# Optimization experiments

Hardware: AMD Instinct MI355X
Metric: run time of the kernel (lower is better)

Reference implementation:

```python
import jax, jax.numpy as jnp
import numpy as np
import math

B, H, S, D = 2, 16, 2048, 64

def setup_inputs() -> dict:
    key = jax.random.key(0)
    kq, kk, kv = jax.random.split(key, 3)
    Q = jax.random.normal(kq, (B, H, S, D), dtype=jnp.float32)
    K = jax.random.normal(kk, (B, H, S, D), dtype=jnp.float32)
    V = jax.random.normal(kv, (B, H, S, D), dtype=jnp.float32)
    causal_mask = jnp.tril(jnp.ones((S, S), dtype=bool))
    return {"Q": Q, "K": K, "V": V, "causal_mask": causal_mask}

def reference(Q, K, V, causal_mask):
    d_k = K.shape[-1]
    scores = jnp.einsum('bhqd,bhkd->bhqk', Q, K) / math.sqrt(d_k)
    scores = jnp.where(causal_mask, scores, -jnp.inf)
    probs = jax.nn.softmax(scores, axis=-1)
    return jnp.einsum('bhqk,bhkd->bhqd', probs, V)
```

## Files before the change

kernel.cpp:

```cpp
#include <hip/hip_runtime.h>
#include <math.h>


constexpr int kS   = 2048;
constexpr int kD   = 64;
constexpr int kBH  = 32;
constexpr int kPadP = 72;

typedef short short8 __attribute__((ext_vector_type(8)));
typedef float float4v __attribute__((ext_vector_type(4)));
typedef float float16v __attribute__((ext_vector_type(16)));
typedef unsigned int u32;
typedef unsigned short u16;

static __device__ inline u16 f2bf(float f) {
  union { float f; unsigned u; } v; v.f = f;
  unsigned r = v.u + 0x7FFF + ((v.u >> 16) & 1);
  return (u16)(r >> 16);
}

static __device__ inline short8 pack8(float4v a, float4v b) {
  short8 r;
  r[0] = (short)f2bf(a[0]); r[1] = (short)f2bf(a[1]);
  r[2] = (short)f2bf(a[2]); r[3] = (short)f2bf(a[3]);
  r[4] = (short)f2bf(b[0]); r[5] = (short)f2bf(b[1]);
  r[6] = (short)f2bf(b[2]); r[7] = (short)f2bf(b[3]);
  return r;
}

static __device__ inline void async_cp16(const void* g, void* l) {
  __builtin_amdgcn_global_load_lds(
      (const __attribute__((address_space(1))) u32*)g,
      (__attribute__((address_space(3))) u32*)l, 16, 0, 0);
}

static __device__ inline void xhalf(u32 pga, u32 pgb, u32& lo, u32& hi) {
#if __has_builtin(__builtin_amdgcn_permlane32_swap)
  auto r = __builtin_amdgcn_permlane32_swap(pga, pgb, false, false);
  lo = r[0];
  hi = r[1];
#else
  const u32 ea = (u32)__shfl_xor((int)pga, 32);
  const u32 eb = (u32)__shfl_xor((int)pgb, 32);
  const bool top = (threadIdx.x & 32) != 0;
  lo = top ? eb : pga;
  hi = top ? pgb : ea;
#endif
}

__global__ __launch_bounds__(256)
void prep_kernel(const float* __restrict__ Q, const float* __restrict__ K,
                 const float* __restrict__ V,
                 u16* __restrict__ Qb, u16* __restrict__ Kb, u16* __restrict__ VT) {
  __shared__ u16 tile[64 * kPadP];
  const int tid = threadIdx.x;
  const int bh = blockIdx.y, st = blockIdx.x;
  const size_t ibase = (size_t)bh * kS * kD + (size_t)st * 64 * kD;
  const int r  = tid >> 2;
  const int c0 = (tid & 3) * 16;
  {
    const float scl = 0.125f * 1.44269504089f;
    const float* qp = Q + ibase + (size_t)r * kD + c0;
    float4v a = *(const float4v*)(qp);
    float4v b = *(const float4v*)(qp + 4);
    float4v c = *(const float4v*)(qp + 8);
    float4v d = *(const float4v*)(qp + 12);
    #pragma unroll
    for (int i = 0; i < 4; ++i) { a[i] *= scl; b[i] *= scl; c[i] *= scl; d[i] *= scl; }
    u16* dst = Qb + ibase + (size_t)r * kD + c0;
    *(short8*)dst       = pack8(a, b);
    *(short8*)(dst + 8) = pack8(c, d);
  }
  {
    const float* kp = K + ibase + (size_t)r * kD + c0;
    float4v a = *(const float4v*)(kp);
    float4v b = *(const float4v*)(kp + 4);
    float4v c = *(const float4v*)(kp + 8);
    float4v d = *(const float4v*)(kp + 12);
    u16* dst = Kb + ibase + (size_t)r * kD + c0;
    *(short8*)dst       = pack8(a, b);
    *(short8*)(dst + 8) = pack8(c, d);
  }
  {
    const float* vp = V + ibase + (size_t)r * kD + c0;
    float4v a = *(const float4v*)(vp);
    float4v b = *(const float4v*)(vp + 4);
    float4v c = *(const float4v*)(vp + 8);
    float4v d = *(const float4v*)(vp + 12);
    u16* t = &tile[r * kPadP + c0];
    *(short8*)t       = pack8(a, b);
    *(short8*)(t + 8) = pack8(c, d);
  }
  __syncthreads();
  {
    const int dd = tid >> 2;
    const int s0 = (tid & 3) * 16;
    short8 w0, w1;
    #pragma unroll
    for (int i = 0; i < 8; ++i) {
      w0[i] = (short)tile[(s0 + i) * kPadP + dd];
      w1[i] = (short)tile[(s0 + 8 + i) * kPadP + dd];
    }
    u16* vdst = VT + (size_t)bh * kD * kS + (size_t)dd * kS + st * 64 + s0;
    *(short8*)vdst       = w0;
    *(short8*)(vdst + 8) = w1;
  }
}

__global__ __launch_bounds__(256, 2)
void fattn_kernel(const u16* __restrict__ Qb, const u16* __restrict__ Kb,
                  const u16* __restrict__ VT,
                  u32* __restrict__ O0, u32* __restrict__ O1,
                  u32* __restrict__ O2, u32* __restrict__ O3,
                  float* __restrict__ Lp) {
  __shared__ __align__(16) u16 ldsK[2][4096];
  __shared__ __align__(16) u16 ldsV[2][4096];

  const int tid  = threadIdx.x;
  const int wave = tid >> 6;
  const int lane = tid & 63;
  const int l31  = lane & 31;
  const int h    = lane >> 5;

  const int bh = blockIdx.y;
  const int p  = blockIdx.x >> 2;
  const int z  = blockIdx.x & 3;
  const int qiA = p, qiB = 7 - p;
  const int nA  = 4 * p + 4;

  const size_t base  = (size_t)bh * kS * kD;
  const size_t vbase = (size_t)bh * kD * kS;

  const int lr  = lane >> 3;
  const int cxl = (lane & 7) ^ lr;
  const int offK0 = lr * 64   + cxl * 8;
  const int offV0 = lr * 2048 + cxl * 8;
  const unsigned hs16 = ((unsigned)(h ^ (l31 & 7))) * 16;

  u32* Od = (z == 0) ? O0 : (z == 1) ? O1 : (z == 2) ? O2 : O3;
  const int cB = 9 * z;
  const int cE = cB + 9;

  short8 ones;
  #pragma unroll
  for (int i = 0; i < 8; ++i) ones[i] = (short)0x3F80;

  int par = 0;
  for (int seg = 0; seg < 2; ++seg) {
    const int qi = seg ? qiB : qiA;
    int tb, te;
    if (seg == 0) { tb = min(cB, nA); te = min(cE, nA); }
    else          { tb = max(cB, nA) - nA; te = max(cE, nA) - nA; }
    const int wq0 = qi * 256 + wave * 64;

    short8 qf[2][4];
    #pragma unroll
    for (int g = 0; g < 2; ++g) {
      const u16* qp = Qb + base + (size_t)(wq0 + 32 * g + l31) * kD + h * 8;
      #pragma unroll
      for (int dk = 0; dk < 4; ++dk) qf[g][dk] = *(const short8*)(qp + dk * 16);
    }

    float16v acc[2][2], lacc[2];
    #pragma unroll
    for (int g = 0; g < 2; ++g) {
      #pragma unroll
      for (int i = 0; i < 16; ++i) { acc[g][0][i] = 0.f; acc[g][1][i] = 0.f; lacc[g][i] = 0.f; }
    }

    if (tb < te) {
      {
        const u16* kg0 = Kb + base + (size_t)tb * 4096;
        const u16* vg0 = VT + vbase + tb * 64;
        const int b = par & 1;
        #pragma unroll
        for (int j = 0; j < 2; ++j) {
          const int g = wave + 4 * j;
          async_cp16(kg0 + g * 512 + offK0,           &ldsK[b][g * 512]);
          async_cp16(vg0 + (size_t)g * 16384 + offV0, &ldsV[b][g * 512]);
        }
      }
      for (int t = tb; t < te; ++t, ++par) {
        __syncthreads();
        if (t + 1 < te) {
          const u16* kg0 = Kb + base + (size_t)(t + 1) * 4096;
          const u16* vg0 = VT + vbase + (t + 1) * 64;
          const int b = (par + 1) & 1;
          #pragma unroll
          for (int j = 0; j < 2; ++j) {
            const int g = wave + 4 * j;
            async_cp16(kg0 + g * 512 + offK0,           &ldsK[b][g * 512]);
            async_cp16(vg0 + (size_t)g * 16384 + offV0, &ldsV[b][g * 512]);
          }
        }
        const char* KB = (const char*)ldsK[par & 1];
        const char* VB = (const char*)ldsV[par & 1];
        #pragma unroll
        for (int kt32 = 0; kt32 < 2; ++kt32) {
          const int ktb = t * 64 + kt32 * 32;
          if (ktb > wq0 + 63) break;
          const bool live0 = (ktb <= wq0 + 31);

          const char* krow = KB + (kt32 * 32 + l31) * 128;
          short8 kf[4];
          #pragma unroll
          for (int dk = 0; dk < 4; ++dk)
            kf[dk] = *(const short8*)(krow + (((unsigned)(dk * 32)) ^ hs16));
          short8 vf[4];
          #pragma unroll
          for (int c = 0; c < 2; ++c) {
            const unsigned coff = ((unsigned)((kt32 * 4 + 2 * c) * 16)) ^ hs16;
            vf[2 * c]     = *(const short8*)(VB + l31 * 128 + coff);
            vf[2 * c + 1] = *(const short8*)(VB + (32 + l31) * 128 + coff);
          }

          float16v s0, s1;
          #pragma unroll
          for (int i = 0; i < 16; ++i) { s0[i] = 0.f; s1[i] = 0.f; }
          if (live0) {
            #pragma unroll
            for (int dk = 0; dk < 4; ++dk)
              s0 = __builtin_amdgcn_mfma_f32_32x32x16_bf16(kf[dk], qf[0][dk], s0, 0, 0, 0);
          }
          #pragma unroll
          for (int dk = 0; dk < 4; ++dk)
            s1 = __builtin_amdgcn_mfma_f32_32x32x16_bf16(kf[dk], qf[1][dk], s1, 0, 0, 0);

          #pragma unroll
          for (int g = 0; g < 2; ++g) {
            if (g == 0 && !live0) continue;
            float16v& s = g ? s1 : s0;

            if (ktb == wq0 + 32 * g) {
              const int qg = wq0 + 32 * g + l31;
              #pragma unroll
              for (int r = 0; r < 16; ++r) {
                const int kg = ktb + (r & 3) + 8 * (r >> 2) + 4 * h;
                if (kg > qg) s[r] = -1e30f;
              }
            }

            u32 pk[8];
            #pragma unroll
            for (int g2 = 0; g2 < 4; ++g2) {
              const u32 u0 = __float_as_uint(__builtin_amdgcn_exp2f(s[4 * g2 + 0]));
              const u32 u1 = __float_as_uint(__builtin_amdgcn_exp2f(s[4 * g2 + 1]));
              const u32 u2 = __float_as_uint(__builtin_amdgcn_exp2f(s[4 * g2 + 2]));
              const u32 u3 = __float_as_uint(__builtin_amdgcn_exp2f(s[4 * g2 + 3]));
              pk[2 * g2]     = __builtin_amdgcn_perm(u1, u0, 0x07060302u);
              pk[2 * g2 + 1] = __builtin_amdgcn_perm(u3, u2, 0x07060302u);
            }

            #pragma unroll
            for (int c = 0; c < 2; ++c) {
              const int ga = 4 * c, gb = 4 * c + 2;
              union { u32 u[4]; short8 s8; } pf;
              xhalf(pk[ga],     pk[gb],     pf.u[0], pf.u[2]);
              xhalf(pk[ga + 1], pk[gb + 1], pf.u[1], pf.u[3]);
              acc[g][0] = __builtin_amdgcn_mfma_f32_32x32x16_bf16(pf.s8, vf[2 * c],     acc[g][0], 0, 0, 0);
              acc[g][1] = __builtin_amdgcn_mfma_f32_32x32x16_bf16(pf.s8, vf[2 * c + 1], acc[g][1], 0, 0, 0);
              lacc[g]   = __builtin_amdgcn_mfma_f32_32x32x16_bf16(pf.s8, ones,          lacc[g],   0, 0, 0);
            }
          }
        }
      }
    }

    #pragma unroll
    for (int g = 0; g < 2; ++g) {
      #pragma unroll
      for (int r = 0; r < 16; ++r) {
        const int row = (r & 3) + 8 * (r >> 2) + 4 * h;
        const u32 w = (u32)f2bf(acc[g][0][r]) | ((u32)f2bf(acc[g][1][r]) << 16);
        Od[((size_t)bh * kS + wq0 + 32 * g + row) * 32 + l31] = w;
      }
      if (l31 == 0) {
        #pragma unroll
        for (int r = 0; r < 16; ++r) {
          const int row = (r & 3) + 8 * (r >> 2) + 4 * h;
          Lp[(size_t)z * kBH * kS + (size_t)bh * kS + wq0 + 32 * g + row] = lacc[g][r];
        }
      }
    }
  }
}

__global__ __launch_bounds__(256)
void combine_kernel(const u32* __restrict__ O0, const u32* __restrict__ O1,
                    const u32* __restrict__ O2, const u32* __restrict__ O3,
                    const float* __restrict__ Lp, float* __restrict__ O) {
  const int idx = blockIdx.x * 256 + threadIdx.x;
  const int row = idx >> 5;
  const int j   = idx & 31;
  const int N = kBH * kS;
  const float l = Lp[row] + Lp[N + row] + Lp[2 * N + row] + Lp[3 * N + row];
  const float inv = 1.f / l;
  const u32 a = O0[idx], b = O1[idx], c = O2[idx], d = O3[idx];
  const float lo = __uint_as_float(a << 16) + __uint_as_float(b << 16)
                 + __uint_as_float(c << 16) + __uint_as_float(d << 16);
  const float hi = __uint_as_float(a & 0xFFFF0000u) + __uint_as_float(b & 0xFFFF0000u)
                 + __uint_as_float(c & 0xFFFF0000u) + __uint_as_float(d & 0xFFFF0000u);
  float* op = O + (size_t)row * kD;
  op[j]      = lo * inv;
  op[j + 32] = hi * inv;
}

extern "C" void kernel_launch(void* const* d_in, const int* in_sizes, int n_in,
                              void* d_out, int out_size, void* d_ws, size_t ws_size,
                              hipStream_t stream) {
  const float* Q = (const float*)d_in[0];
  const float* K = (const float*)d_in[1];
  const float* V = (const float*)d_in[2];
  float* O = (float*)d_out;

  const size_t nKV = (size_t)kBH * kS * kD;
  u16* Qb = (u16*)d_ws;
  u16* Kb = Qb + nKV;
  u16* VT = Kb + nKV;
  u32* O0 = (u32*)(VT + nKV);
  u32* O1 = O0 + nKV / 2;
  u32* O2 = O1 + nKV / 2;
  u32* O3 = O2 + nKV / 2;
  float* Lp = (float*)(O3 + nKV / 2);

  dim3 gprep(kS / 64, kBH);
  prep_kernel<<<gprep, 256, 0, stream>>>(Q, K, V, Qb, Kb, VT);
  dim3 grid(16, kBH);
  fattn_kernel<<<grid, 256, 0, stream>>>(Qb, Kb, VT, O0, O1, O2, O3, Lp);
  combine_kernel<<<(int)(kBH * kS * 32 / 256), 256, 0, stream>>>(O0, O1, O2, O3, Lp, O);
}
```

Measured before the change: 146.0 us.

## Split KV range into eight chunks per paired query tile, raise occupancy

The KV-chunk split factor per paired (qiA, qiB) block goes from 4 to 8, using uneven constant begin/end tables. This doubles the grid to 32x32 blocks and raises launch_bounds occupancy to 4 blocks per CU, aiming for better load balance and latency hiding on the many CUs. Blocks whose segment is empty now skip it, and the combine kernel sums only the partials that contributed. The cost is more partial-output traffic and more combine work, plus register pressure from the higher occupancy target.

```diff
diff --git a/kernel.cpp b/kernel.cpp
--- a/kernel.cpp
+++ b/kernel.cpp
@@ -6,6 +6,10 @@
 constexpr int kD   = 64;
 constexpr int kBH  = 32;
 constexpr int kPadP = 72;
+constexpr int kNZ  = 8;
+
+__device__ __constant__ const int kCB[8] = {0, 4, 9, 13, 18, 22, 27, 31};
+__device__ __constant__ const int kCE[8] = {4, 9, 13, 18, 22, 27, 31, 36};
 
 typedef short short8 __attribute__((ext_vector_type(8)));
 typedef float float4v __attribute__((ext_vector_type(4)));
@@ -107,12 +111,10 @@
   }
 }
 
-__global__ __launch_bounds__(256, 2)
+__global__ __launch_bounds__(256, 4)
 void fattn_kernel(const u16* __restrict__ Qb, const u16* __restrict__ Kb,
                   const u16* __restrict__ VT,
-                  u32* __restrict__ O0, u32* __restrict__ O1,
-                  u32* __restrict__ O2, u32* __restrict__ O3,
-                  float* __restrict__ Lp) {
+                  u32* __restrict__ Op, float* __restrict__ Lp) {
   __shared__ __align__(16) u16 ldsK[2][4096];
   __shared__ __align__(16) u16 ldsV[2][4096];
 
@@ -123,13 +125,14 @@
   const int h    = lane >> 5;
 
   const int bh = blockIdx.y;
-  const int p  = blockIdx.x >> 2;
-  const int z  = blockIdx.x & 3;
+  const int p  = blockIdx.x >> 3;
+  const int z  = blockIdx.x & 7;
   const int qiA = p, qiB = 7 - p;
   const int nA  = 4 * p + 4;
 
   const size_t base  = (size_t)bh * kS * kD;
   const size_t vbase = (size_t)bh * kD * kS;
+  const size_t nO    = (size_t)kBH * kS * 32;
 
   const int lr  = lane >> 3;
   const int cxl = (lane & 7) ^ lr;
@@ -137,9 +140,9 @@
   const int offV0 = lr * 2048 + cxl * 8;
   const unsigned hs16 = ((unsigned)(h ^ (l31 & 7))) * 16;
 
-  u32* Od = (z == 0) ? O0 : (z == 1) ? O1 : (z == 2) ? O2 : O3;
-  const int cB = 9 * z;
-  const int cE = cB + 9;
+  u32* Od = Op + (size_t)z * nO;
+  const int cB = kCB[z];
+  const int cE = kCE[z];
 
   short8 ones;
   #pragma unroll
@@ -151,6 +154,8 @@
     int tb, te;
     if (seg == 0) { tb = min(cB, nA); te = min(cE, nA); }
     else          { tb = max(cB, nA) - nA; te = max(cE, nA) - nA; }
+    if (tb >= te) continue;
+
     const int wq0 = qi * 256 + wave * 64;
 
     short8 qf[2][4];
@@ -168,11 +173,23 @@
       for (int i = 0; i < 16; ++i) { acc[g][0][i] = 0.f; acc[g][1][i] = 0.f; lacc[g][i] = 0.f; }
     }
 
-    if (tb < te) {
-      {
-        const u16* kg0 = Kb + base + (size_t)tb * 4096;
-        const u16* vg0 = VT + vbase + tb * 64;
-        const int b = par & 1;
+    {
+      const u16* kg0 = Kb + base + (size_t)tb * 4096;
+      const u16* vg0 = VT + vbase + tb * 64;
+      const int b = par & 1;
+      #pragma unroll
+      for (int j = 0; j < 2; ++j) {
+        const int g = wave + 4 * j;
+        async_cp16(kg0 + g * 512 + offK0,           &ldsK[b][g * 512]);
+        async_cp16(vg0 + (size_t)g * 16384 + offV0, &ldsV[b][g * 512]);
+      }
+    }
+    for (int t = tb; t < te; ++t, ++par) {
+      __syncthreads();
+      if (t + 1 < te) {
+        const u16* kg0 = Kb + base + (size_t)(t + 1) * 4096;
+        const u16* vg0 = VT + vbase + (t + 1) * 64;
+        const int b = (par + 1) & 1;
         #pragma unroll
         for (int j = 0; j < 2; ++j) {
           const int g = wave + 4 * j;
@@ -180,91 +197,78 @@
           async_cp16(vg0 + (size_t)g * 16384 + offV0, &ldsV[b][g * 512]);
         }
       }
-      for (int t = tb; t < te; ++t, ++par) {
-        __syncthreads();
-        if (t + 1 < te) {
-          const u16* kg0 = Kb + base + (size_t)(t + 1) * 4096;
-          const u16* vg0 = VT + vbase + (t + 1) * 64;
-          const int b = (par + 1) & 1;
-          #pragma unroll
-          for (int j = 0; j < 2; ++j) {
-            const int g = wave + 4 * j;
-            async_cp16(kg0 + g * 512 + offK0,           &ldsK[b][g * 512]);
-            async_cp16(vg0 + (size_t)g * 16384 + offV0, &ldsV[b][g * 512]);
-          }
-        }
-        const char* KB = (const char*)ldsK[par & 1];
-        const char* VB = (const char*)ldsV[par & 1];
-        #pragma unroll
-        for (int kt32 = 0; kt32 < 2; ++kt32) {
-          const int ktb = t * 64 + kt32 * 32;
-          if (ktb > wq0 + 63) break;
-          const bool live0 = (ktb <= wq0 + 31);
-
-          const char* krow = KB + (kt32 * 32 + l31) * 128;
-          short8 kf[4];
+      const char* KB = (const char*)ldsK[par & 1];
+      const char* VB = (const char*)ldsV[par & 1];
+      #pragma unroll
+      for (int kt32 = 0; kt32 < 2; ++kt32) {
+        const int ktb = t * 64 + kt32 * 32;
+        if (ktb > wq0 + 63) break;
+        const bool live0 = (ktb <= wq0 + 31);
+
+        const char* krow = KB + (kt32 * 32 + l31) * 128;
+        short8 kf[4];
+        #pragma unroll
+        for (int dk = 0; dk < 4; ++dk)
+          kf[dk] = *(const short8*)(krow + (((unsigned)(dk * 32)) ^ hs16));
+        short8 vf[4];
+        #pragma unroll
+        for (int c = 0; c < 2; ++c) {
+          const unsigned coff = ((unsigned)((kt32 * 4 + 2 * c) * 16)) ^ hs16;
+          vf[2 * c]     = *(const short8*)(VB + l31 * 128 + coff);
+          vf[2 * c + 1] = *(const short8*)(VB + (32 + l31) * 128 + coff);
+        }
+
+        float16v s0, s1;
+        #pragma unroll
+        for (int i = 0; i < 16; ++i) { s0[i] = 0.f; s1[i] = 0.f; }
+        if (live0) {
           #pragma unroll
           for (int dk = 0; dk < 4; ++dk)
-            kf[dk] = *(const short8*)(krow + (((unsigned)(dk * 32)) ^ hs16));
-          short8 vf[4];
+            s0 = __builtin_amdgcn_mfma_f32_32x32x16_bf16(kf[dk], qf[0][dk], s0, 0, 0, 0);
+        }
+        #pragma unroll
+        for (int dk = 0; dk < 4; ++dk)
+          s1 = __builtin_amdgcn_mfma_f32_32x32x16_bf16(kf[dk], qf[1][dk], s1, 0, 0, 0);
+
+        #pragma unroll
+        for (int g = 0; g < 2; ++g) {
+          if (g == 0 && !live0) continue;
+          float16v& s = g ? s1 : s0;
+
+          if (ktb == wq0 + 32 * g) {
+            const int qg = wq0 + 32 * g + l31;
+            #pragma unroll
+            for (int r = 0; r < 16; ++r) {
+              const int kg = ktb + (r & 3) + 8 * (r >> 2) + 4 * h;
+              if (kg > qg) s[r] = -1e30f;
+            }
+          }
+
+          u32 pk[8];
+          #pragma unroll
+          for (int g2 = 0; g2 < 4; ++g2) {
+            const u32 u0 = __float_as_uint(__builtin_amdgcn_exp2f(s[4 * g2 + 0]));
+            const u32 u1 = __float_as_uint(__builtin_amdgcn_exp2f(s[4 * g2 + 1]));
+            const u32 u2 = __float_as_uint(__builtin_amdgcn_exp2f(s[4 * g2 + 2]));
+            const u32 u3 = __float_as_uint(__builtin_amdgcn_exp2f(s[4 * g2 + 3]));
+            pk[2 * g2]     = __builtin_amdgcn_perm(u1, u0, 0x07060302u);
+            pk[2 * g2 + 1] = __builtin_amdgcn_perm(u3, u2, 0x07060302u);
+          }
+
           #pragma unroll
           for (int c = 0; c < 2; ++c) {
-            const unsigned coff = ((unsigned)((kt32 * 4 + 2 * c) * 16)) ^ hs16;
-            vf[2 * c]     = *(const short8*)(VB + l31 * 128 + coff);
-            vf[2 * c + 1] = *(const short8*)(VB + (32 + l31) * 128 + coff);
+            const int ga = 4 * c, gb = 4 * c + 2;
+            union { u32 u[4]; short8 s8; } pf;
+            xhalf(pk[ga],     pk[gb],     pf.u[0], pf.u[2]);
+            xhalf(pk[ga + 1], pk[gb + 1], pf.u[1], pf.u[3]);
+            acc[g][0] = __builtin_amdgcn_mfma_f32_32x32x16_bf16(pf.s8, vf[2 * c],     acc[g][0], 0, 0, 0);
+            acc[g][1] = __builtin_amdgcn_mfma_f32_32x32x16_bf16(pf.s8, vf[2 * c + 1], acc[g][1], 0, 0, 0);
+            lacc[g]   = __builtin_amdgcn_mfma_f32_32x32x16_bf16(pf.s8, ones,          lacc[g],   0, 0, 0);
           }
-
-          float16v s0, s1;
-          #pragma unroll
-          for (int i = 0; i < 16; ++i) { s0[i] = 0.f; s1[i] = 0.f; }
-          if (live0) {
-            #pragma unroll
-            for (int dk = 0; dk < 4; ++dk)
-              s0 = __builtin_amdgcn_mfma_f32_32x32x16_bf16(kf[dk], qf[0][dk], s0, 0, 0, 0);
-          }
-          #pragma unroll
-          for (int dk = 0; dk < 4; ++dk)
-            s1 = __builtin_amdgcn_mfma_f32_32x32x16_bf16(kf[dk], qf[1][dk], s1, 0, 0, 0);
-
-          #pragma unroll
-          for (int g = 0; g < 2; ++g) {
-            if (g == 0 && !live0) continue;
-            float16v& s = g ? s1 : s0;
-
-            if (ktb == wq0 + 32 * g) {
-              const int qg = wq0 + 32 * g + l31;
-              #pragma unroll
-              for (int r = 0; r < 16; ++r) {
-                const int kg = ktb + (r & 3) + 8 * (r >> 2) + 4 * h;
-                if (kg > qg) s[r] = -1e30f;
-              }
-            }
-
-            u32 pk[8];
-            #pragma unroll
-            for (int g2 = 0; g2 < 4; ++g2) {
-              const u32 u0 = __float_as_uint(__builtin_amdgcn_exp2f(s[4 * g2 + 0]));
-              const u32 u1 = __float_as_uint(__builtin_amdgcn_exp2f(s[4 * g2 + 1]));
-              const u32 u2 = __float_as_uint(__builtin_amdgcn_exp2f(s[4 * g2 + 2]));
-              const u32 u3 = __float_as_uint(__builtin_amdgcn_exp2f(s[4 * g2 + 3]));
-              pk[2 * g2]     = __builtin_amdgcn_perm(u1, u0, 0x07060302u);
-              pk[2 * g2 + 1] = __builtin_amdgcn_perm(u3, u2, 0x07060302u);
-            }
-
-            #pragma unroll
-            for (int c = 0; c < 2; ++c) {
-              const int ga = 4 * c, gb = 4 * c + 2;
-              union { u32 u[4]; short8 s8; } pf;
-              xhalf(pk[ga],     pk[gb],     pf.u[0], pf.u[2]);
-              xhalf(pk[ga + 1], pk[gb + 1], pf.u[1], pf.u[3]);
-              acc[g][0] = __builtin_amdgcn_mfma_f32_32x32x16_bf16(pf.s8, vf[2 * c],     acc[g][0], 0, 0, 0);
-              acc[g][1] = __builtin_amdgcn_mfma_f32_32x32x16_bf16(pf.s8, vf[2 * c + 1], acc[g][1], 0, 0, 0);
-              lacc[g]   = __builtin_amdgcn_mfma_f32_32x32x16_bf16(pf.s8, ones,          lacc[g],   0, 0, 0);
-            }
-          }
-        }
-      }
-    }
+        }
+      }
+    }
+    __syncthreads();
 
     #pragma unroll
     for (int g = 0; g < 2; ++g) {
@@ -286,20 +290,27 @@
 }
 
 __global__ __launch_bounds__(256)
-void combine_kernel(const u32* __restrict__ O0, const u32* __restrict__ O1,
-                    const u32* __restrict__ O2, const u32* __restrict__ O3,
-                    const float* __restrict__ Lp, float* __restrict__ O) {
+void combine_kernel(const u32* __restrict__ Op, const float* __restrict__ Lp,
+                    float* __restrict__ O) {
   const int idx = blockIdx.x * 256 + threadIdx.x;
   const int row = idx >> 5;
   const int j   = idx & 31;
-  const int N = kBH * kS;
-  const float l = Lp[row] + Lp[N + row] + Lp[2 * N + row] + Lp[3 * N + row];
+  const int N  = kBH * kS;
+  const size_t nO = (size_t)N * 32;
+  const int qi = (row >> 8) & 7;
+
+  float l = 0.f, lo = 0.f, hi = 0.f;
+  #pragma unroll
+  for (int z = 0; z < kNZ; ++z) {
+    const bool contrib = (qi <= 3) ? (kCB[z] < 4 * qi + 4) : (kCE[z] > 32 - 4 * qi);
+    if (contrib) {
+      l += Lp[(size_t)z * N + row];
+      const u32 a = Op[(size_t)z * nO + idx];
+      lo += __uint_as_float(a << 16);
+      hi += __uint_as_float(a & 0xFFFF0000u);
+    }
+  }
   const float inv = 1.f / l;
-  const u32 a = O0[idx], b = O1[idx], c = O2[idx], d = O3[idx];
-  const float lo = __uint_as_float(a << 16) + __uint_as_float(b << 16)
-                 + __uint_as_float(c << 16) + __uint_as_float(d << 16);
-  const float hi = __uint_as_float(a & 0xFFFF0000u) + __uint_as_float(b & 0xFFFF0000u)
-                 + __uint_as_float(c & 0xFFFF0000u) + __uint_as_float(d & 0xFFFF0000u);
   float* op = O + (size_t)row * kD;
   op[j]      = lo * inv;
   op[j + 32] = hi * inv;
@@ -317,15 +328,12 @@
   u16* Qb = (u16*)d_ws;
   u16* Kb = Qb + nKV;
   u16* VT = Kb + nKV;
-  u32* O0 = (u32*)(VT + nKV);
-  u32* O1 = O0 + nKV / 2;
-  u32* O2 = O1 + nKV / 2;
-  u32* O3 = O2 + nKV / 2;
-  float* Lp = (float*)(O3 + nKV / 2);
+  u32* Op = (u32*)(VT + nKV);
+  float* Lp = (float*)(Op + (size_t)kNZ * nKV / 2);
 
   dim3 gprep(kS / 64, kBH);
   prep_kernel<<<gprep, 256, 0, stream>>>(Q, K, V, Qb, Kb, VT);
-  dim3 grid(16, kBH);
-  fattn_kernel<<<grid, 256, 0, stream>>>(Qb, Kb, VT, O0, O1, O2, O3, Lp);
-  combine_kernel<<<(int)(kBH * kS * 32 / 256), 256, 0, stream>>>(O0, O1, O2, O3, Lp, O);
-}
+  dim3 grid(4 * kNZ, kBH);
+  fattn_kernel<<<grid, 256, 0, stream>>>(Qb, Kb, VT, Op, Lp);
+  combine_kernel<<<(int)(kBH * kS * 32 / 256), 256, 0, stream>>>(Op, Lp, O);
+}
```

Result: slower. 367.2 us (+151.5%).
